# Kernel tuning notes

Measured on AMD Instinct MI355X. Metric: run time of the kernel, lower is better.

## Reference

```python
import jax, jax.numpy as jnp
import numpy as np

V, D, H, KV, L, FF, HD = 32000, 768, 12, 4, 4, 2048, 64
N_REP = H // KV  # 3
EPS = 1e-6
ROPE_THETA = 10000.0


def setup_inputs() -> dict:
    key = jax.random.key(0)
    ks = jax.random.split(key, 12)
    s = 0.02
    return {
        'idx': jax.random.randint(ks[0], (1, 2048), 0, V),
        'embed': jax.random.normal(ks[1], (V, D), jnp.float32) * s,
        'ln1_w': jnp.ones((L, D), jnp.float32),
        'Wq': jax.random.normal(ks[2], (L, D, H * HD), jnp.float32) * s,
        'Wk': jax.random.normal(ks[3], (L, D, KV * HD), jnp.float32) * s,
        'Wv': jax.random.normal(ks[4], (L, D, KV * HD), jnp.float32) * s,
        'Wo': jax.random.normal(ks[5], (L, H * HD, D), jnp.float32) * s,
        'ln2_w': jnp.ones((L, D), jnp.float32),
        'Wg': jax.random.normal(ks[6], (L, D, FF), jnp.float32) * s,
        'Wu': jax.random.normal(ks[7], (L, D, FF), jnp.float32) * s,
        'Wd': jax.random.normal(ks[8], (L, FF, D), jnp.float32) * s,
        'normf_w': jnp.ones((D,), jnp.float32),
    }


def _rms(x, w):
    xf = x.astype(jnp.float32)
    var = jnp.mean(xf * xf, axis=-1, keepdims=True)
    return w * (xf * jax.lax.rsqrt(var + EPS)).astype(x.dtype)


def _rotate_half(x):
    x1, x2 = x[..., : x.shape[-1] // 2], x[..., x.shape[-1] // 2:]
    return jnp.concatenate((-x2, x1), axis=-1)


def reference(idx, embed, ln1_w, Wq, Wk, Wv, Wo, ln2_w, Wg, Wu, Wd, normf_w):
    B, T = idx.shape
    x = embed[idx]  # [B,T,D]

    # RoPE tables: cos/sin [1,1,T,HD]
    inv_freq = 1.0 / (ROPE_THETA ** (jnp.arange(0, HD, 2, dtype=jnp.float32) / HD))
    pos = jnp.arange(T, dtype=jnp.float32)
    freqs = pos[:, None] * inv_freq[None, :]          # [T,HD/2]
    emb = jnp.concatenate((freqs, freqs), axis=-1)     # [T,HD]
    cos = jnp.cos(emb)[None, None].astype(x.dtype)
    sin = jnp.sin(emb)[None, None].astype(x.dtype)

    causal = jnp.tril(jnp.ones((T, T), bool))[None, None]  # [1,1,T,T]
    scale = 1.0 / np.sqrt(HD)

    for l in range(L):
        # --- attention ---
        h = _rms(x, ln1_w[l])
        q = (h @ Wq[l]).reshape(B, T, H, HD).transpose(0, 2, 1, 3)   # [B,H,T,HD]
        k = (h @ Wk[l]).reshape(B, T, KV, HD).transpose(0, 2, 1, 3)  # [B,KV,T,HD]
        v = (h @ Wv[l]).reshape(B, T, KV, HD).transpose(0, 2, 1, 3)
        q = q * cos + _rotate_half(q) * sin
        k = k * cos + _rotate_half(k) * sin
        k = jnp.repeat(k, N_REP, axis=1)  # [B,H,T,HD]
        v = jnp.repeat(v, N_REP, axis=1)
        scores = jnp.einsum('bhqd,bhkd->bhqk', q, k) * scale
        scores = jnp.where(causal, scores, -jnp.inf)
        probs = jax.nn.softmax(scores.astype(jnp.float32), axis=-1).astype(q.dtype)
        attn = jnp.einsum('bhqk,bhkd->bhqd', probs, v)
        attn = attn.transpose(0, 2, 1, 3).reshape(B, T, H * HD)
        x = x + attn @ Wo[l]
        # --- gated MLP ---
        h = _rms(x, ln2_w[l])
        x = x + (jax.nn.gelu(h @ Wg[l], approximate=True) * (h @ Wu[l])) @ Wd[l]

    x = _rms(x, normf_w)
    logits = (x @ embed.T).astype(jnp.float32)  # tied lm_head
    return logits
```

## Files before the change

### kernel.cpp

```cpp
#include <hip/hip_runtime.h>

#define TSEQ 2048
#define DM   768
#define NH   12
#define NKV  4
#define HD   64
#define FFD  2048
#define NL   4
#define VOC  32000
#define QKVN 1280

typedef __attribute__((ext_vector_type(8))) short short8;
typedef __attribute__((ext_vector_type(4))) float f32x4;

__device__ __forceinline__ unsigned short f2b(float f) {
  unsigned int u = __float_as_uint(f);
  u += 0x7fffu + ((u >> 16) & 1u);
  return (unsigned short)(u >> 16);
}
__device__ __forceinline__ float b2f(unsigned short u) {
  return __uint_as_float(((unsigned int)u) << 16);
}
__device__ __forceinline__ unsigned int packbf(float a, float b) {
  return (unsigned int)f2b(a) | ((unsigned int)f2b(b) << 16);
}

__device__ __forceinline__ void gl16(const unsigned short* g, unsigned short* l) {
  __builtin_amdgcn_global_load_lds(
      (const __attribute__((address_space(1))) void*)g,
      (__attribute__((address_space(3))) void*)l, 16, 0, 0);
}

__global__ void cast_bf16_kernel(const float* __restrict__ src,
                                 unsigned short* __restrict__ dst, int n4) {
  int i = blockIdx.x * blockDim.x + threadIdx.x;
  if (i >= n4) return;
  float4 v = ((const float4*)src)[i];
  uint2 o; o.x = packbf(v.x, v.y); o.y = packbf(v.z, v.w);
  ((uint2*)dst)[i] = o;
}

__global__ void rope_tab_kernel(float2* __restrict__ tab) {
  int i = blockIdx.x * blockDim.x + threadIdx.x;
  int pos = i >> 5, d = i & 31;
  float inv = exp2f(-(float)d * (13.287712379549449f / 32.0f));
  float sv, cv; sincosf((float)pos * inv, &sv, &cv);
  tab[i] = make_float2(cv, sv);
}

__global__ void transpose_cast_kernel(const float* __restrict__ src,
                                      unsigned short* __restrict__ dst,
                                      int K, int N, size_t sstride, size_t dstride) {
  __shared__ float tile[32][33];
  src += (size_t)blockIdx.z * sstride;
  dst += (size_t)blockIdx.z * dstride;
  int n0 = blockIdx.x * 32, k0 = blockIdx.y * 32;
  int tx = threadIdx.x, ty = threadIdx.y;
  #pragma unroll
  for (int i = 0; i < 4; ++i) {
    int r = ty + i * 8;
    tile[r][tx] = src[(size_t)(k0 + r) * N + n0 + tx];
  }
  __syncthreads();
  #pragma unroll
  for (int i = 0; i < 4; ++i) {
    int r = ty + i * 8;
    dst[(size_t)(n0 + r) * K + k0 + tx] = f2b(tile[tx][r]);
  }
}

__global__ void gather_kernel(const int* __restrict__ idx,
                              const float* __restrict__ embed,
                              float* __restrict__ x) {
  int row = blockIdx.x; int t = threadIdx.x;
  int id = idx[row];
  ((float4*)(x + (size_t)row * DM))[t] = ((const float4*)(embed + (size_t)id * DM))[t];
}

__global__ void rmsnorm_kernel(const float* __restrict__ x,
                               const float* __restrict__ w,
                               unsigned short* __restrict__ out) {
  int row = blockIdx.x; int t = threadIdx.x;
  const float* xr = x + (size_t)row * DM;
  float v0 = xr[t], v1 = xr[t + 256], v2 = xr[t + 512];
  float s = v0*v0 + v1*v1 + v2*v2;
  #pragma unroll
  for (int off = 1; off < 64; off <<= 1) s += __shfl_xor(s, off);
  __shared__ float red[4];
  if ((t & 63) == 0) red[t >> 6] = s;
  __syncthreads();
  float tot = red[0] + red[1] + red[2] + red[3];
  float rs = rsqrtf(tot * (1.0f / DM) + 1e-6f);
  unsigned short* orow = out + (size_t)row * DM;
  orow[t]       = f2b(w[t]       * v0 * rs);
  orow[t + 256] = f2b(w[t + 256] * v1 * rs);
  orow[t + 512] = f2b(w[t + 512] * v2 * rs);
}

__global__ __launch_bounds__(512, 1) void gemm_l8_kernel(
    const unsigned short* __restrict__ A, const unsigned short* __restrict__ Bt,
    float* __restrict__ C, int N, int K) {
  __shared__ unsigned short lds[2][2][256 * 64];
  const int NT = K >> 6;
  int bid = blockIdx.x, nwg = gridDim.x;
  int wgid = (bid & 7) * (nwg >> 3) + (bid >> 3);
  int m0 = (wgid & 7) * 256;
  int n0 = (wgid >> 3) * 256;
  int tid = threadIdx.x;
  int lane = tid & 63, w = tid >> 6;
  int wm = w >> 2, wn = w & 3;
  int al = lane & 15, ag = lane >> 4;
  int swz = (al & 7) << 3;

  int rA = tid >> 3;
  int cK = ((tid & 7) * 8) ^ ((rA & 7) << 3);
  const unsigned short* Ag = A + (size_t)(m0 + rA) * K + cK;
  const unsigned short* Bg = Bt + (size_t)(n0 + rA) * K + cK;

  f32x4 acc[8][4];
  #pragma unroll
  for (int i = 0; i < 8; ++i)
    #pragma unroll
    for (int n = 0; n < 4; ++n) acc[i][n] = (f32x4){0.f, 0.f, 0.f, 0.f};

  #define STAGE(kt, c) { \
    size_t ko = (size_t)(kt) * 64; \
    unsigned short* dA = &lds[(c)][0][0] + w * 512; \
    unsigned short* dB = &lds[(c)][1][0] + w * 512; \
    gl16(Ag + (size_t)0   * K + ko, dA);            \
    gl16(Ag + (size_t)64  * K + ko, dA + 4096);     \
    gl16(Ag + (size_t)128 * K + ko, dA + 8192);     \
    gl16(Ag + (size_t)192 * K + ko, dA + 12288);    \
    gl16(Bg + (size_t)0   * K + ko, dB);            \
    gl16(Bg + (size_t)64  * K + ko, dB + 4096);     \
    gl16(Bg + (size_t)128 * K + ko, dB + 8192);     \
    gl16(Bg + (size_t)192 * K + ko, dB + 12288);    \
  }

  STAGE(0, 0);
  STAGE(1, 1);
  asm volatile("s_waitcnt vmcnt(8)" ::: "memory");
  __builtin_amdgcn_s_barrier();

  for (int t = 0; t < NT; ++t) {
    int cur = t & 1;
    const unsigned short* La = &lds[cur][0][0];
    const unsigned short* Lb = &lds[cur][1][0];
    short8 a0[8], b0[4], a1[8], b1[4];
    #pragma unroll
    for (int i = 0; i < 8; ++i)
      a0[i] = *(const short8*)&La[(wm*128 + i*16 + al)*64 + ((ag*8) ^ swz)];
    #pragma unroll
    for (int n = 0; n < 4; ++n)
      b0[n] = *(const short8*)&Lb[(wn*64 + n*16 + al)*64 + ((ag*8) ^ swz)];
    #pragma unroll
    for (int i = 0; i < 8; ++i)
      #pragma unroll
      for (int n = 0; n < 4; ++n)
        acc[i][n] = __builtin_amdgcn_mfma_f32_16x16x32_bf16(a0[i], b0[n], acc[i][n], 0, 0, 0);
    #pragma unroll
    for (int i = 0; i < 8; ++i)
      a1[i] = *(const short8*)&La[(wm*128 + i*16 + al)*64 + ((32 + ag*8) ^ swz)];
    #pragma unroll
    for (int n = 0; n < 4; ++n)
      b1[n] = *(const short8*)&Lb[(wn*64 + n*16 + al)*64 + ((32 + ag*8) ^ swz)];
    asm volatile("s_waitcnt lgkmcnt(0)" ::: "memory");
    __builtin_amdgcn_s_barrier();
    if (t + 2 < NT) STAGE(t + 2, cur);
    __builtin_amdgcn_s_setprio(1);
    #pragma unroll
    for (int i = 0; i < 8; ++i)
      #pragma unroll
      for (int n = 0; n < 4; ++n)
        acc[i][n] = __builtin_amdgcn_mfma_f32_16x16x32_bf16(a1[i], b1[n], acc[i][n], 0, 0, 0);
    __builtin_amdgcn_s_setprio(0);
    if (t + 2 < NT) { asm volatile("s_waitcnt vmcnt(8)" ::: "memory"); }
    else            { asm volatile("s_waitcnt vmcnt(0)" ::: "memory"); }
    __builtin_amdgcn_s_barrier();
  }
  #undef STAGE

  #pragma unroll
  for (int i = 0; i < 8; ++i)
    #pragma unroll
    for (int r = 0; r < 4; ++r) {
      float* Cr = C + (size_t)(m0 + wm*128 + i*16 + ag*4 + r) * N + n0 + wn*64 + al;
      #pragma unroll
      for (int n = 0; n < 4; ++n) Cr[n * 16] = acc[i][n][r];
    }
}

__global__ __launch_bounds__(512) void gemm_p8_kernel(
    const unsigned short* __restrict__ A, const unsigned short* __restrict__ Bt,
    float* __restrict__ C, int N, int K, int Kc) {
  __shared__ unsigned short lds[2][2][128 * 64];
  const int NT = Kc >> 6;
  int bid = blockIdx.x, nwg = gridDim.x;
  int wgid = (bid & 7) * (nwg >> 3) + (bid >> 3);
  int m0 = (wgid & 15) * 128;
  int n0 = (wgid >> 4) * 128;
  int tid = threadIdx.x;
  int lane = tid & 63, w = tid >> 6;
  int wm = w >> 2, wn = w & 3;
  int al = lane & 15, ag = lane >> 4;
  int swz = (al & 7) << 3;

  size_t koff = (size_t)blockIdx.y * Kc;
  int rp = 8 * w + (lane >> 3);
  int cK = ((lane & 7) * 8) ^ ((lane >> 3) << 3);
  const unsigned short* Ag = A + (size_t)(m0 + rp) * K + koff + cK;
  const unsigned short* Bg = Bt + (size_t)(n0 + rp) * K + koff + cK;

  f32x4 acc[4][2];
  #pragma unroll
  for (int i = 0; i < 4; ++i)
    #pragma unroll
    for (int n = 0; n < 2; ++n) acc[i][n] = (f32x4){0.f, 0.f, 0.f, 0.f};

  #define STAGE(kt, c) { \
    size_t ko = (size_t)(kt) * 64; \
    unsigned short* dA = &lds[(c)][0][0] + w * 512; \
    unsigned short* dB = &lds[(c)][1][0] + w * 512; \
    gl16(Ag + ko,                 dA);        \
    gl16(Ag + (size_t)64*K + ko,  dA + 4096); \
    gl16(Bg + ko,                 dB);        \
    gl16(Bg + (size_t)64*K + ko,  dB + 4096); \
  }

  STAGE(0, 0);
  STAGE(1, 1);
  asm volatile("s_waitcnt vmcnt(4)" ::: "memory");
  __builtin_amdgcn_s_barrier();

  for (int t = 0; t < NT; ++t) {
    int cur = t & 1;
    const unsigned short* La = &lds[cur][0][0];
    const unsigned short* Lb = &lds[cur][1][0];
    short8 a0[4], b0[2], a1[4], b1[2];
    #pragma unroll
    for (int i = 0; i < 4; ++i)
      a0[i] = *(const short8*)&La[(wm*64 + i*16 + al)*64 + ((ag*8) ^ swz)];
    #pragma unroll
    for (int n = 0; n < 2; ++n)
      b0[n] = *(const short8*)&Lb[(wn*32 + n*16 + al)*64 + ((ag*8) ^ swz)];
    #pragma unroll
    for (int i = 0; i < 4; ++i)
      #pragma unroll
      for (int n = 0; n < 2; ++n)
        acc[i][n] = __builtin_amdgcn_mfma_f32_16x16x32_bf16(a0[i], b0[n], acc[i][n], 0, 0, 0);
    #pragma unroll
    for (int i = 0; i < 4; ++i)
      a1[i] = *(const short8*)&La[(wm*64 + i*16 + al)*64 + ((32 + ag*8) ^ swz)];
    #pragma unroll
    for (int n = 0; n < 2; ++n)
      b1[n] = *(const short8*)&Lb[(wn*32 + n*16 + al)*64 + ((32 + ag*8) ^ swz)];
    asm volatile("s_waitcnt lgkmcnt(0)" ::: "memory");
    __builtin_amdgcn_s_barrier();
    if (t + 2 < NT) STAGE(t + 2, cur);
    __builtin_amdgcn_s_setprio(1);
    #pragma unroll
    for (int i = 0; i < 4; ++i)
      #pragma unroll
      for (int n = 0; n < 2; ++n)
        acc[i][n] = __builtin_amdgcn_mfma_f32_16x16x32_bf16(a1[i], b1[n], acc[i][n], 0, 0, 0);
    __builtin_amdgcn_s_setprio(0);
    if (t + 2 < NT) { asm volatile("s_waitcnt vmcnt(4)" ::: "memory"); }
    else            { asm volatile("s_waitcnt vmcnt(0)" ::: "memory"); }
    __builtin_amdgcn_s_barrier();
  }
  #undef STAGE

  #pragma unroll
  for (int i = 0; i < 4; ++i)
    #pragma unroll
    for (int r = 0; r < 4; ++r) {
      float* Cr = C + (size_t)(m0 + wm*64 + i*16 + ag*4 + r) * N + n0 + wn*32 + al;
      #pragma unroll
      for (int n = 0; n < 2; ++n) atomicAdd(&Cr[n * 16], acc[i][n][r]);
    }
}

__device__ __forceinline__ float gelu_t(float x) {
  float x3 = x * x * x;
  return 0.5f * x * (1.0f + tanhf(0.7978845608028654f * (x + 0.044715f * x3)));
}

__global__ __launch_bounds__(512) void gemm_gu8_kernel(
    const unsigned short* __restrict__ A, const unsigned short* __restrict__ BtG,
    const unsigned short* __restrict__ BtU, unsigned short* __restrict__ Cm) {
  __shared__ unsigned short lds[2][3][128 * 64];
  const int K = DM;
  const int NT = K >> 6;
  int bid = blockIdx.x, nwg = gridDim.x;
  int wgid = (bid & 7) * (nwg >> 3) + (bid >> 3);
  int m0 = (wgid & 15) * 128;
  int n0 = (wgid >> 4) * 128;
  int tid = threadIdx.x;
  int lane = tid & 63, w = tid >> 6;
  int wm = w >> 2, wn = w & 3;
  int al = lane & 15, ag = lane >> 4;
  int swz = (al & 7) << 3;

  int rp = 8 * w + (lane >> 3);
  int cK = ((lane & 7) * 8) ^ ((lane >> 3) << 3);
  const unsigned short* Ag = A + (size_t)(m0 + rp) * K + cK;
  const unsigned short* Gg = BtG + (size_t)(n0 + rp) * K + cK;
  const unsigned short* Ug = BtU + (size_t)(n0 + rp) * K + cK;

  f32x4 accg[4][2], accu[4][2];
  #pragma unroll
  for (int i = 0; i < 4; ++i)
    #pragma unroll
    for (int n = 0; n < 2; ++n) {
      accg[i][n] = (f32x4){0.f, 0.f, 0.f, 0.f};
      accu[i][n] = (f32x4){0.f, 0.f, 0.f, 0.f};
    }

  #define STAGE(kt, c) { \
    size_t ko = (size_t)(kt) * 64; \
    unsigned short* dA = &lds[(c)][0][0] + w * 512; \
    unsigned short* dG = &lds[(c)][1][0] + w * 512; \
    unsigned short* dU = &lds[(c)][2][0] + w * 512; \
    gl16(Ag + ko,                 dA);        \
    gl16(Ag + (size_t)64*K + ko,  dA + 4096); \
    gl16(Gg + ko,                 dG);        \
    gl16(Gg + (size_t)64*K + ko,  dG + 4096); \
    gl16(Ug + ko,                 dU);        \
    gl16(Ug + (size_t)64*K + ko,  dU + 4096); \
  }

  STAGE(0, 0);
  STAGE(1, 1);
  asm volatile("s_waitcnt vmcnt(6)" ::: "memory");
  __builtin_amdgcn_s_barrier();

  for (int t = 0; t < NT; ++t) {
    int cur = t & 1;
    const unsigned short* La = &lds[cur][0][0];
    const unsigned short* Lg = &lds[cur][1][0];
    const unsigned short* Lu = &lds[cur][2][0];
    short8 a0[4], g0[2], u0[2], a1[4], g1[2], u1[2];
    #pragma unroll
    for (int i = 0; i < 4; ++i)
      a0[i] = *(const short8*)&La[(wm*64 + i*16 + al)*64 + ((ag*8) ^ swz)];
    #pragma unroll
    for (int n = 0; n < 2; ++n) {
      g0[n] = *(const short8*)&Lg[(wn*32 + n*16 + al)*64 + ((ag*8) ^ swz)];
      u0[n] = *(const short8*)&Lu[(wn*32 + n*16 + al)*64 + ((ag*8) ^ swz)];
    }
    #pragma unroll
    for (int i = 0; i < 4; ++i)
      #pragma unroll
      for (int n = 0; n < 2; ++n) {
        accg[i][n] = __builtin_amdgcn_mfma_f32_16x16x32_bf16(a0[i], g0[n], accg[i][n], 0, 0, 0);
        accu[i][n] = __builtin_amdgcn_mfma_f32_16x16x32_bf16(a0[i], u0[n], accu[i][n], 0, 0, 0);
      }
    #pragma unroll
    for (int i = 0; i < 4; ++i)
      a1[i] = *(const short8*)&La[(wm*64 + i*16 + al)*64 + ((32 + ag*8) ^ swz)];
    #pragma unroll
    for (int n = 0; n < 2; ++n) {
      g1[n] = *(const short8*)&Lg[(wn*32 + n*16 + al)*64 + ((32 + ag*8) ^ swz)];
      u1[n] = *(const short8*)&Lu[(wn*32 + n*16 + al)*64 + ((32 + ag*8) ^ swz)];
    }
    asm volatile("s_waitcnt lgkmcnt(0)" ::: "memory");
    __builtin_amdgcn_s_barrier();
    if (t + 2 < NT) STAGE(t + 2, cur);
    __builtin_amdgcn_s_setprio(1);
    #pragma unroll
    for (int i = 0; i < 4; ++i)
      #pragma unroll
      for (int n = 0; n < 2; ++n) {
        accg[i][n] = __builtin_amdgcn_mfma_f32_16x16x32_bf16(a1[i], g1[n], accg[i][n], 0, 0, 0);
        accu[i][n] = __builtin_amdgcn_mfma_f32_16x16x32_bf16(a1[i], u1[n], accu[i][n], 0, 0, 0);
      }
    __builtin_amdgcn_s_setprio(0);
    if (t + 2 < NT) { asm volatile("s_waitcnt vmcnt(6)" ::: "memory"); }
    else            { asm volatile("s_waitcnt vmcnt(0)" ::: "memory"); }
    __builtin_amdgcn_s_barrier();
  }
  #undef STAGE

  #pragma unroll
  for (int i = 0; i < 4; ++i)
    #pragma unroll
    for (int r = 0; r < 4; ++r) {
      unsigned short* Cr = Cm + (size_t)(m0 + wm*64 + i*16 + ag*4 + r) * FFD + n0 + wn*32 + al;
      #pragma unroll
      for (int n = 0; n < 2; ++n)
        Cr[n * 16] = f2b(gelu_t(accg[i][n][r]) * accu[i][n][r]);
    }
}

__global__ __launch_bounds__(256) void gemm_qkv_kernel(
    const unsigned short* __restrict__ A, const unsigned short* __restrict__ Bt,
    unsigned short* __restrict__ C, unsigned short* __restrict__ vT,
    const float2* __restrict__ rope_tab) {
  const int N = QKVN, K = DM;
  __shared__ unsigned short As[128 * 40];
  __shared__ unsigned short Bs[128 * 40];
  int bid = blockIdx.x, nwg = gridDim.x;
  int wgid = (bid & 7) * (nwg >> 3) + (bid >> 3);
  int m0 = (wgid & 15) * 128;
  int n0 = (wgid >> 4) * 128;
  int tid = threadIdx.x;
  int lane = tid & 63, wave = tid >> 6;
  int wr = (wave >> 1) * 64, wc = (wave & 1) * 64;
  int l16 = lane & 15, lk8 = (lane >> 4) * 8;
  f32x4 acc[4][4];
  #pragma unroll
  for (int m = 0; m < 4; ++m)
    #pragma unroll
    for (int n = 0; n < 4; ++n) acc[m][n] = (f32x4){0.f, 0.f, 0.f, 0.f};
  const unsigned short* Abase = A + (size_t)m0 * K;
  const unsigned short* Bbase = Bt + (size_t)n0 * K;
  int r0 = tid >> 2;
  int c0 = (tid & 3) * 8;
  for (int k0 = 0; k0 < K; k0 += 32) {
    uint4 a0 = *(const uint4*)(Abase + (size_t)r0 * K + k0 + c0);
    uint4 a1 = *(const uint4*)(Abase + (size_t)(r0 + 64) * K + k0 + c0);
    uint4 b0 = *(const uint4*)(Bbase + (size_t)r0 * K + k0 + c0);
    uint4 b1 = *(const uint4*)(Bbase + (size_t)(r0 + 64) * K + k0 + c0);
    *(uint4*)&As[r0 * 40 + c0] = a0;
    *(uint4*)&As[(r0 + 64) * 40 + c0] = a1;
    *(uint4*)&Bs[r0 * 40 + c0] = b0;
    *(uint4*)&Bs[(r0 + 64) * 40 + c0] = b1;
    __syncthreads();
    short8 af[4], bfr[4];
    #pragma unroll
    for (int m = 0; m < 4; ++m) af[m]  = *(const short8*)&As[(wr + m*16 + l16) * 40 + lk8];
    #pragma unroll
    for (int n = 0; n < 4; ++n) bfr[n] = *(const short8*)&Bs[(wc + n*16 + l16) * 40 + lk8];
    #pragma unroll
    for (int m = 0; m < 4; ++m)
      #pragma unroll
      for (int n = 0; n < 4; ++n)
        acc[m][n] = __builtin_amdgcn_mfma_f32_16x16x32_bf16(af[m], bfr[n], acc[m][n], 0, 0, 0);
    __syncthreads();
  }
  bool qk = (n0 + wc) < 1024;
  #pragma unroll
  for (int m = 0; m < 4; ++m)
    #pragma unroll
    for (int r = 0; r < 4; ++r) {
      int pos = m0 + wr + m*16 + ((lane >> 4) << 2) + r;
      if (qk) {
        unsigned short* Cr = C + (size_t)pos * N + n0 + wc + l16;
        #pragma unroll
        for (int n = 0; n < 2; ++n) {
          int d = n * 16 + l16;
          float2 cs = rope_tab[pos * 32 + d];
          float x1 = acc[m][n][r], x2 = acc[m][n + 2][r];
          Cr[n * 16]       = f2b(x1 * cs.x - x2 * cs.y);
          Cr[(n + 2) * 16] = f2b(x2 * cs.x + x1 * cs.y);
        }
      } else {
        #pragma unroll
        for (int n = 0; n < 4; ++n) {
          int hb = n0 + wc + n*16 + l16 - 1024;
          vT[(size_t)hb * TSEQ + pos] = f2b(acc[m][n][r]);
        }
      }
    }
}

__global__ __launch_bounds__(256) void attn_chunk_kernel(
    const unsigned short* __restrict__ qkv, const unsigned short* __restrict__ vT,
    unsigned short* __restrict__ out, float* __restrict__ pO, float* __restrict__ pML) {
  __shared__ unsigned short Ks[2][64 * 64];
  __shared__ unsigned short Vt[2][64 * 64];
  __shared__ unsigned short Ps[4][16 * 64];
  int s = blockIdx.x, h = blockIdx.y;
  int qt, ci;
  if (s < 8)       { qt = s;                ci = 0; }
  else if (s < 24) { qt = 8 + ((s-8) >> 1); ci = (s-8) & 1; }
  else if (s < 48) { qt = 16 + (s-24) / 3;  ci = (s-24) % 3; }
  else             { qt = 24 + ((s-48) >> 2); ci = (s-48) & 3; }
  int nt = qt + 1;
  int t0 = ci * 8;
  int t1 = t0 + 8; if (t1 > nt) t1 = nt;
  int cnt = (nt + 7) >> 3;
  int r0 = qt * 64;
  int kvh = h / 3;
  int t = threadIdx.x;
  int lane = t & 63, w = t >> 6;
  int l16 = lane & 15, g = lane >> 4;

  int qr = r0 + w * 16 + l16;
  const unsigned short* qrow = qkv + (size_t)qr * QKVN + h * HD;
  short8 aq0 = *(const short8*)(qrow + 8 * g);
  short8 aq1 = *(const short8*)(qrow + 32 + 8 * g);

  int sw = (lane & 7) ^ (lane >> 3);
  int rloc = w * 16 + (lane >> 3);
  const unsigned short* kgb = qkv + (size_t)rloc * QKVN + DM + kvh * HD + 8 * sw;
  const unsigned short* vgb = vT + (size_t)(kvh * 64 + rloc) * TSEQ + 8 * sw;

  #define ASTAGE(kb, c) { \
    unsigned short* kd = &Ks[(c)][0] + w * 1024; \
    unsigned short* vd = &Vt[(c)][0] + w * 1024; \
    gl16(kgb + (size_t)(kb) * QKVN,       kd);       \
    gl16(kgb + (size_t)((kb) + 8) * QKVN, kd + 512); \
    gl16(vgb + (kb),                      vd);       \
    gl16(vgb + (size_t)8 * TSEQ + (kb),   vd + 512); \
  }

  f32x4 o_acc[4];
  float mrun[4], lsum[4];
  #pragma unroll
  for (int i = 0; i < 4; ++i) { o_acc[i] = (f32x4){0.f,0.f,0.f,0.f}; mrun[i] = -1e30f; lsum[i] = 0.f; }

  ASTAGE(t0 * 64, 0);
  for (int kt = t0; kt < t1; ++kt) {
    int cur = (kt - t0) & 1;
    int kb = kt * 64;
    if (kt + 1 < t1) {
      ASTAGE((kt + 1) * 64, cur ^ 1);
      asm volatile("s_waitcnt vmcnt(4)" ::: "memory");
    } else {
      asm volatile("s_waitcnt vmcnt(0)" ::: "memory");
    }
    __builtin_amdgcn_s_barrier();

    const unsigned short* Kc = &Ks[cur][0];
    const unsigned short* Vc = &Vt[cur][0];

    f32x4 s_acc[4];
    #pragma unroll
    for (int nb = 0; nb < 4; ++nb) s_acc[nb] = (f32x4){0.f,0.f,0.f,0.f};
    #pragma unroll
    for (int nb = 0; nb < 4; ++nb) {
      int key = nb * 16 + l16;
      short8 bk0 = *(const short8*)&Kc[key * 64 + ((g       ^ (key & 7)) << 3)];
      short8 bk1 = *(const short8*)&Kc[key * 64 + (((4 + g) ^ (key & 7)) << 3)];
      s_acc[nb] = __builtin_amdgcn_mfma_f32_16x16x32_bf16(aq0, bk0, s_acc[nb], 0, 0, 0);
      s_acc[nb] = __builtin_amdgcn_mfma_f32_16x16x32_bf16(aq1, bk1, s_acc[nb], 0, 0, 0);
    }

    bool diag = (kt == qt);
    #pragma unroll
    for (int r = 0; r < 4; ++r) {
      int qg = r0 + w * 16 + g * 4 + r;
      float sv[4];
      #pragma unroll
      for (int nb = 0; nb < 4; ++nb) {
        sv[nb] = s_acc[nb][r] * 0.125f;
        if (diag && (kb + nb * 16 + l16 > qg)) sv[nb] = -1e30f;
      }
      float mx = fmaxf(fmaxf(sv[0], sv[1]), fmaxf(sv[2], sv[3]));
      mx = fmaxf(mx, __shfl_xor(mx, 1));
      mx = fmaxf(mx, __shfl_xor(mx, 2));
      mx = fmaxf(mx, __shfl_xor(mx, 4));
      mx = fmaxf(mx, __shfl_xor(mx, 8));
      if (mx > mrun[r] + 8.0f) {
        float es = __expf(mrun[r] - mx);
        lsum[r] *= es;
        #pragma unroll
        for (int db = 0; db < 4; ++db) o_acc[db][r] *= es;
        mrun[r] = mx;
      }
      float rsum = 0.f;
      #pragma unroll
      for (int nb = 0; nb < 4; ++nb) { sv[nb] = __expf(sv[nb] - mrun[r]); rsum += sv[nb]; }
      lsum[r] += rsum;
      int qloc = g * 4 + r, q7 = qloc & 7;
      #pragma unroll
      for (int nb = 0; nb < 4; ++nb) {
        int key = nb * 16 + l16;
        Ps[w][qloc * 64 + ((((key >> 3) ^ q7) << 3) + (key & 7))] = f2b(sv[nb]);
      }
    }

    #pragma unroll
    for (int kc = 0; kc < 2; ++kc) {
      short8 pa = *(const short8*)&Ps[w][l16 * 64 + (((4 * kc + g) ^ (l16 & 7)) << 3)];
      #pragma unroll
      for (int db = 0; db < 4; ++db) {
        int d = db * 16 + l16;
        short8 bv = *(const short8*)&Vc[d * 64 + (((4 * kc + g) ^ (d & 7)) << 3)];
        o_acc[db] = __builtin_amdgcn_mfma_f32_16x16x32_bf16(pa, bv, o_acc[db], 0, 0, 0);
      }
    }
    __builtin_amdgcn_s_barrier();
  }
  #undef ASTAGE

  if (cnt == 1) {
    #pragma unroll
    for (int r = 0; r < 4; ++r) {
      int qg = r0 + w * 16 + g * 4 + r;
      float sr = lsum[r];
      sr += __shfl_xor(sr, 1);
      sr += __shfl_xor(sr, 2);
      sr += __shfl_xor(sr, 4);
      sr += __shfl_xor(sr, 8);
      float inv = 1.0f / sr;
      unsigned short* orow = out + (size_t)qg * DM + h * HD + l16;
      #pragma unroll
      for (int db = 0; db < 4; ++db) orow[db * 16] = f2b(o_acc[db][r] * inv);
    }
  } else {
    size_t slotg = (size_t)h * 80 + s;
    float* po = pO + slotg * 4096;
    float* pm = pML + slotg * 128;
    #pragma unroll
    for (int r = 0; r < 4; ++r) {
      int row = w * 16 + g * 4 + r;
      float sr = lsum[r];
      sr += __shfl_xor(sr, 1);
      sr += __shfl_xor(sr, 2);
      sr += __shfl_xor(sr, 4);
      sr += __shfl_xor(sr, 8);
      #pragma unroll
      for (int db = 0; db < 4; ++db) po[row * 64 + db * 16 + l16] = o_acc[db][r];
      if (l16 == 0) { pm[row * 2] = mrun[r]; pm[row * 2 + 1] = sr; }
    }
  }
}

__global__ __launch_bounds__(256) void attn_combine_kernel(
    const float* __restrict__ pO, const float* __restrict__ pML,
    unsigned short* __restrict__ out) {
  int h = blockIdx.y;
  int qt = 8 + blockIdx.x;
  int base, cnt;
  if (qt < 16)      { base = 8 + (qt - 8) * 2;  cnt = 2; }
  else if (qt < 24) { base = 24 + (qt - 16) * 3; cnt = 3; }
  else              { base = 48 + (qt - 24) * 4; cnt = 4; }
  int t = threadIdx.x;
  int row = t >> 2, d0 = (t & 3) * 16;
  float m[4], l[4];
  float M = -1e30f;
  for (int c = 0; c < cnt; ++c) {
    const float* pm = pML + ((size_t)h * 80 + base + c) * 128 + row * 2;
    m[c] = pm[0]; l[c] = pm[1];
    M = fmaxf(M, m[c]);
  }
  float o[16];
  #pragma unroll
  for (int j = 0; j < 16; ++j) o[j] = 0.f;
  float wl = 0.f;
  for (int c = 0; c < cnt; ++c) {
    float wc = __expf(m[c] - M);
    wl += wc * l[c];
    const float4* po = (const float4*)(pO + ((size_t)h * 80 + base + c) * 4096 + row * 64 + d0);
    #pragma unroll
    for (int q = 0; q < 4; ++q) {
      float4 v = po[q];
      o[q*4+0] += wc * v.x; o[q*4+1] += wc * v.y;
      o[q*4+2] += wc * v.z; o[q*4+3] += wc * v.w;
    }
  }
  float inv = 1.0f / wl;
  unsigned short* orow = out + (size_t)(qt * 64 + row) * DM + h * HD + d0;
  uint4 s0, s1;
  s0.x = packbf(o[0]*inv,  o[1]*inv);  s0.y = packbf(o[2]*inv,  o[3]*inv);
  s0.z = packbf(o[4]*inv,  o[5]*inv);  s0.w = packbf(o[6]*inv,  o[7]*inv);
  s1.x = packbf(o[8]*inv,  o[9]*inv);  s1.y = packbf(o[10]*inv, o[11]*inv);
  s1.z = packbf(o[12]*inv, o[13]*inv); s1.w = packbf(o[14]*inv, o[15]*inv);
  ((uint4*)orow)[0] = s0; ((uint4*)orow)[1] = s1;
}

extern "C" void kernel_launch(void* const* d_in, const int* in_sizes, int n_in,
                              void* d_out, int out_size, void* d_ws, size_t ws_size,
                              hipStream_t stream) {
  const int*   idx   = (const int*)d_in[0];
  const float* embed = (const float*)d_in[1];
  const float* ln1   = (const float*)d_in[2];
  const float* Wq    = (const float*)d_in[3];
  const float* Wk    = (const float*)d_in[4];
  const float* Wv    = (const float*)d_in[5];
  const float* Wo    = (const float*)d_in[6];
  const float* ln2   = (const float*)d_in[7];
  const float* Wg    = (const float*)d_in[8];
  const float* Wu    = (const float*)d_in[9];
  const float* Wd    = (const float*)d_in[10];
  const float* normf = (const float*)d_in[11];
  float* out = (float*)d_out;
  char* ws = (char*)d_ws;
  (void)in_sizes; (void)n_in; (void)out_size; (void)ws_size;

  unsigned short* embed_bf = (unsigned short*)ws;
  size_t off = (size_t)VOC * DM * 2;
  unsigned short* wts = (unsigned short*)(ws + off);
  const size_t LW = (size_t)QKVN * DM + (size_t)DM * DM
                  + 2ull * FFD * DM + (size_t)DM * FFD;
  off += LW * 2ull * NL;
  float* xf = (float*)(ws + off);            off += (size_t)TSEQ * DM * 4;
  unsigned short* h_bf = (unsigned short*)(ws + off);    off += (size_t)TSEQ * DM * 2;
  unsigned short* qkv_bf = (unsigned short*)(ws + off);  off += (size_t)TSEQ * QKVN * 2;
  unsigned short* attn_bf = (unsigned short*)(ws + off); off += (size_t)TSEQ * DM * 2;
  float* pO = (float*)(ws + off);
  unsigned short* m_bf = (unsigned short*)(ws + off);
  off += (size_t)NH * 80 * 4096 * 4;
  float* pML = (float*)(ws + off);           off += (size_t)NH * 80 * 128 * 4;
  float2* rope_tab = (float2*)(ws + off);    off += (size_t)TSEQ * 32 * 8;
  unsigned short* vT = (unsigned short*)(ws + off);      off += (size_t)NKV * HD * TSEQ * 2;

  cast_bf16_kernel<<<(VOC * DM / 4 + 255) / 256, 256, 0, stream>>>(embed, embed_bf, VOC * DM / 4);
  rope_tab_kernel<<<TSEQ * 32 / 256, 256, 0, stream>>>(rope_tab);

  {
    unsigned short* qkvT = wts;
    unsigned short* woT  = wts + (size_t)QKVN * DM;
    unsigned short* wguT = woT + (size_t)DM * DM;
    unsigned short* wdT  = wguT + 2ull * FFD * DM;
    transpose_cast_kernel<<<dim3(24, 24, NL), dim3(32, 8), 0, stream>>>(Wq, qkvT, 768, 768, 589824, LW);
    transpose_cast_kernel<<<dim3(8, 24, NL),  dim3(32, 8), 0, stream>>>(Wk, qkvT + 768ull * 768, 768, 256, 196608, LW);
    transpose_cast_kernel<<<dim3(8, 24, NL),  dim3(32, 8), 0, stream>>>(Wv, qkvT + 1024ull * 768, 768, 256, 196608, LW);
    transpose_cast_kernel<<<dim3(24, 24, NL), dim3(32, 8), 0, stream>>>(Wo, woT, 768, 768, 589824, LW);
    transpose_cast_kernel<<<dim3(64, 24, NL), dim3(32, 8), 0, stream>>>(Wg, wguT, 768, 2048, 1572864, LW);
    transpose_cast_kernel<<<dim3(64, 24, NL), dim3(32, 8), 0, stream>>>(Wu, wguT + (size_t)FFD * DM, 768, 2048, 1572864, LW);
    transpose_cast_kernel<<<dim3(24, 64, NL), dim3(32, 8), 0, stream>>>(Wd, wdT, 2048, 768, 1572864, LW);
  }

  gather_kernel<<<TSEQ, 192, 0, stream>>>(idx, embed, xf);

  for (int l = 0; l < NL; ++l) {
    unsigned short* base = wts + (size_t)l * LW;
    unsigned short* qkvT = base;
    unsigned short* woT  = base + (size_t)QKVN * DM;
    unsigned short* wguT = woT + (size_t)DM * DM;
    unsigned short* wdT  = wguT + 2ull * FFD * DM;

    rmsnorm_kernel<<<TSEQ, 256, 0, stream>>>(xf, ln1 + (size_t)l * DM, h_bf);
    gemm_qkv_kernel<<<(QKVN / 128) * 16, 256, 0, stream>>>(h_bf, qkvT, qkv_bf, vT, rope_tab);
    attn_chunk_kernel<<<dim3(80, NH), 256, 0, stream>>>(qkv_bf, vT, attn_bf, pO, pML);
    attn_combine_kernel<<<dim3(24, NH), 256, 0, stream>>>(pO, pML, attn_bf);
    gemm_p8_kernel<<<dim3((DM / 128) * 16, 3), 512, 0, stream>>>(attn_bf, woT, xf, DM, DM, 256);
    rmsnorm_kernel<<<TSEQ, 256, 0, stream>>>(xf, ln2 + (size_t)l * DM, h_bf);
    gemm_gu8_kernel<<<(FFD / 128) * 16, 512, 0, stream>>>(h_bf, wguT, wguT + (size_t)FFD * DM, m_bf);
    gemm_p8_kernel<<<dim3((DM / 128) * 16, 4), 512, 0, stream>>>(m_bf, wdT, xf, DM, FFD, 512);
  }

  rmsnorm_kernel<<<TSEQ, 256, 0, stream>>>(xf, normf, h_bf);
  gemm_l8_kernel<<<(VOC / 256) * (TSEQ / 256), 512, 0, stream>>>(h_bf, embed_bf, out, VOC, DM);
}
```

Measured before the change: 769.8 us.

## Merge weight transpose launches and interleave LDS fragment loads with MFMA

Seven per-matrix transpose-cast launches become one kernel that works out which matrix each block handles from its flat block index, which saves launch overhead. The three GEMM kernels' inner loops are reordered so the second half-tile's LDS fragment loads are issued before the first half's MFMAs, with partial lgkmcnt waits and sched_barriers. This is meant to hide LDS latency behind matrix math. It raises register pressure because more fragments are live at once.

```diff
diff --git a/kernel.cpp b/kernel.cpp
--- a/kernel.cpp
+++ b/kernel.cpp
@@ -48,24 +48,39 @@
   tab[i] = make_float2(cv, sv);
 }
 
-__global__ void transpose_cast_kernel(const float* __restrict__ src,
-                                      unsigned short* __restrict__ dst,
-                                      int K, int N, size_t sstride, size_t dstride) {
+__global__ void transpose_all_kernel(const float* __restrict__ Wq, const float* __restrict__ Wk,
+                                     const float* __restrict__ Wv, const float* __restrict__ Wo,
+                                     const float* __restrict__ Wg, const float* __restrict__ Wu,
+                                     const float* __restrict__ Wd, unsigned short* __restrict__ wts,
+                                     size_t LW) {
   __shared__ float tile[32][33];
-  src += (size_t)blockIdx.z * sstride;
-  dst += (size_t)blockIdx.z * dstride;
-  int n0 = blockIdx.x * 32, k0 = blockIdx.y * 32;
+  int r = blockIdx.x, l = blockIdx.z;
+  const float* src; size_t sstr, doff; int K, N, nx;
+  if (r < 576)       { src = Wq; sstr = 589824;  doff = 0;                          K = 768;  N = 768;  nx = 24; }
+  else if (r < 768)  { src = Wk; sstr = 196608;  doff = 768ull * 768;               K = 768;  N = 256;  nx = 8;  r -= 576; }
+  else if (r < 960)  { src = Wv; sstr = 196608;  doff = 1024ull * 768;              K = 768;  N = 256;  nx = 8;  r -= 768; }
+  else if (r < 1536) { src = Wo; sstr = 589824;  doff = (size_t)QKVN * DM;          K = 768;  N = 768;  nx = 24; r -= 960; }
+  else if (r < 3072) { src = Wg; sstr = 1572864; doff = (size_t)QKVN * DM + (size_t)DM * DM;
+                       K = 768;  N = 2048; nx = 64; r -= 1536; }
+  else if (r < 4608) { src = Wu; sstr = 1572864; doff = (size_t)QKVN * DM + (size_t)DM * DM + (size_t)FFD * DM;
+                       K = 768;  N = 2048; nx = 64; r -= 3072; }
+  else               { src = Wd; sstr = 1572864; doff = (size_t)QKVN * DM + (size_t)DM * DM + 2ull * FFD * DM;
+                       K = 2048; N = 768;  nx = 24; r -= 4608; }
+  int bx = r % nx, by = r / nx;
+  src += (size_t)l * sstr;
+  unsigned short* dst = wts + (size_t)l * LW + doff;
+  int n0 = bx * 32, k0 = by * 32;
   int tx = threadIdx.x, ty = threadIdx.y;
   #pragma unroll
   for (int i = 0; i < 4; ++i) {
-    int r = ty + i * 8;
-    tile[r][tx] = src[(size_t)(k0 + r) * N + n0 + tx];
+    int rr = ty + i * 8;
+    tile[rr][tx] = src[(size_t)(k0 + rr) * N + n0 + tx];
   }
   __syncthreads();
   #pragma unroll
   for (int i = 0; i < 4; ++i) {
-    int r = ty + i * 8;
-    dst[(size_t)(n0 + r) * K + k0 + tx] = f2b(tile[tx][r]);
+    int rr = ty + i * 8;
+    dst[(size_t)(n0 + rr) * K + k0 + tx] = f2b(tile[tx][rr]);
   }
 }
 
@@ -148,28 +163,51 @@
     const unsigned short* Lb = &lds[cur][1][0];
     short8 a0[8], b0[4], a1[8], b1[4];
     #pragma unroll
-    for (int i = 0; i < 8; ++i)
+    for (int i = 0; i < 4; ++i)
       a0[i] = *(const short8*)&La[(wm*128 + i*16 + al)*64 + ((ag*8) ^ swz)];
     #pragma unroll
     for (int n = 0; n < 4; ++n)
       b0[n] = *(const short8*)&Lb[(wn*64 + n*16 + al)*64 + ((ag*8) ^ swz)];
     #pragma unroll
-    for (int i = 0; i < 8; ++i)
+    for (int i = 4; i < 8; ++i)
+      a0[i] = *(const short8*)&La[(wm*128 + i*16 + al)*64 + ((ag*8) ^ swz)];
+    asm volatile("s_waitcnt lgkmcnt(4)" ::: "memory");
+    __builtin_amdgcn_sched_barrier(0);
+    #pragma unroll
+    for (int i = 0; i < 4; ++i)
       #pragma unroll
       for (int n = 0; n < 4; ++n)
         acc[i][n] = __builtin_amdgcn_mfma_f32_16x16x32_bf16(a0[i], b0[n], acc[i][n], 0, 0, 0);
     #pragma unroll
-    for (int i = 0; i < 8; ++i)
-      a1[i] = *(const short8*)&La[(wm*128 + i*16 + al)*64 + ((32 + ag*8) ^ swz)];
-    #pragma unroll
     for (int n = 0; n < 4; ++n)
       b1[n] = *(const short8*)&Lb[(wn*64 + n*16 + al)*64 + ((32 + ag*8) ^ swz)];
+    #pragma unroll
+    for (int i = 0; i < 4; ++i)
+      a1[i] = *(const short8*)&La[(wm*128 + i*16 + al)*64 + ((32 + ag*8) ^ swz)];
+    asm volatile("s_waitcnt lgkmcnt(8)" ::: "memory");
+    __builtin_amdgcn_sched_barrier(0);
+    #pragma unroll
+    for (int i = 4; i < 8; ++i)
+      #pragma unroll
+      for (int n = 0; n < 4; ++n)
+        acc[i][n] = __builtin_amdgcn_mfma_f32_16x16x32_bf16(a0[i], b0[n], acc[i][n], 0, 0, 0);
+    #pragma unroll
+    for (int i = 4; i < 8; ++i)
+      a1[i] = *(const short8*)&La[(wm*128 + i*16 + al)*64 + ((32 + ag*8) ^ swz)];
+    asm volatile("s_waitcnt lgkmcnt(4)" ::: "memory");
+    __builtin_amdgcn_sched_barrier(0);
+    #pragma unroll
+    for (int i = 0; i < 4; ++i)
+      #pragma unroll
+      for (int n = 0; n < 4; ++n)
+        acc[i][n] = __builtin_amdgcn_mfma_f32_16x16x32_bf16(a1[i], b1[n], acc[i][n], 0, 0, 0);
     asm volatile("s_waitcnt lgkmcnt(0)" ::: "memory");
+    __builtin_amdgcn_sched_barrier(0);
     __builtin_amdgcn_s_barrier();
     if (t + 2 < NT) STAGE(t + 2, cur);
     __builtin_amdgcn_s_setprio(1);
     #pragma unroll
-    for (int i = 0; i < 8; ++i)
+    for (int i = 4; i < 8; ++i)
       #pragma unroll
       for (int n = 0; n < 4; ++n)
         acc[i][n] = __builtin_amdgcn_mfma_f32_16x16x32_bf16(a1[i], b1[n], acc[i][n], 0, 0, 0);
@@ -245,16 +283,19 @@
       b0[n] = *(const short8*)&Lb[(wn*32 + n*16 + al)*64 + ((ag*8) ^ swz)];
     #pragma unroll
     for (int i = 0; i < 4; ++i)
+      a1[i] = *(const short8*)&La[(wm*64 + i*16 + al)*64 + ((32 + ag*8) ^ swz)];
+    #pragma unroll
+    for (int n = 0; n < 2; ++n)
+      b1[n] = *(const short8*)&Lb[(wn*32 + n*16 + al)*64 + ((32 + ag*8) ^ swz)];
+    asm volatile("s_waitcnt lgkmcnt(6)" ::: "memory");
+    __builtin_amdgcn_sched_barrier(0);
+    #pragma unroll
+    for (int i = 0; i < 4; ++i)
       #pragma unroll
       for (int n = 0; n < 2; ++n)
         acc[i][n] = __builtin_amdgcn_mfma_f32_16x16x32_bf16(a0[i], b0[n], acc[i][n], 0, 0, 0);
-    #pragma unroll
-    for (int i = 0; i < 4; ++i)
-      a1[i] = *(const short8*)&La[(wm*64 + i*16 + al)*64 + ((32 + ag*8) ^ swz)];
-    #pragma unroll
-    for (int n = 0; n < 2; ++n)
-      b1[n] = *(const short8*)&Lb[(wn*32 + n*16 + al)*64 + ((32 + ag*8) ^ swz)];
     asm volatile("s_waitcnt lgkmcnt(0)" ::: "memory");
+    __builtin_amdgcn_sched_barrier(0);
     __builtin_amdgcn_s_barrier();
     if (t + 2 < NT) STAGE(t + 2, cur);
     __builtin_amdgcn_s_setprio(1);
@@ -350,20 +391,23 @@
     }
     #pragma unroll
     for (int i = 0; i < 4; ++i)
+      a1[i] = *(const short8*)&La[(wm*64 + i*16 + al)*64 + ((32 + ag*8) ^ swz)];
+    #pragma unroll
+    for (int n = 0; n < 2; ++n) {
+      g1[n] = *(const short8*)&Lg[(wn*32 + n*16 + al)*64 + ((32 + ag*8) ^ swz)];
+      u1[n] = *(const short8*)&Lu[(wn*32 + n*16 + al)*64 + ((32 + ag*8) ^ swz)];
+    }
+    asm volatile("s_waitcnt lgkmcnt(8)" ::: "memory");
+    __builtin_amdgcn_sched_barrier(0);
+    #pragma unroll
+    for (int i = 0; i < 4; ++i)
       #pragma unroll
       for (int n = 0; n < 2; ++n) {
         accg[i][n] = __builtin_amdgcn_mfma_f32_16x16x32_bf16(a0[i], g0[n], accg[i][n], 0, 0, 0);
         accu[i][n] = __builtin_amdgcn_mfma_f32_16x16x32_bf16(a0[i], u0[n], accu[i][n], 0, 0, 0);
       }
-    #pragma unroll
-    for (int i = 0; i < 4; ++i)
-      a1[i] = *(const short8*)&La[(wm*64 + i*16 + al)*64 + ((32 + ag*8) ^ swz)];
-    #pragma unroll
-    for (int n = 0; n < 2; ++n) {
-      g1[n] = *(const short8*)&Lg[(wn*32 + n*16 + al)*64 + ((32 + ag*8) ^ swz)];
-      u1[n] = *(const short8*)&Lu[(wn*32 + n*16 + al)*64 + ((32 + ag*8) ^ swz)];
-    }
     asm volatile("s_waitcnt lgkmcnt(0)" ::: "memory");
+    __builtin_amdgcn_sched_barrier(0);
     __builtin_amdgcn_s_barrier();
     if (t + 2 < NT) STAGE(t + 2, cur);
     __builtin_amdgcn_s_setprio(1);
@@ -699,20 +743,8 @@
 
   cast_bf16_kernel<<<(VOC * DM / 4 + 255) / 256, 256, 0, stream>>>(embed, embed_bf, VOC * DM / 4);
   rope_tab_kernel<<<TSEQ * 32 / 256, 256, 0, stream>>>(rope_tab);
-
-  {
-    unsigned short* qkvT = wts;
-    unsigned short* woT  = wts + (size_t)QKVN * DM;
-    unsigned short* wguT = woT + (size_t)DM * DM;
-    unsigned short* wdT  = wguT + 2ull * FFD * DM;
-    transpose_cast_kernel<<<dim3(24, 24, NL), dim3(32, 8), 0, stream>>>(Wq, qkvT, 768, 768, 589824, LW);
-    transpose_cast_kernel<<<dim3(8, 24, NL),  dim3(32, 8), 0, stream>>>(Wk, qkvT + 768ull * 768, 768, 256, 196608, LW);
-    transpose_cast_kernel<<<dim3(8, 24, NL),  dim3(32, 8), 0, stream>>>(Wv, qkvT + 1024ull * 768, 768, 256, 196608, LW);
-    transpose_cast_kernel<<<dim3(24, 24, NL), dim3(32, 8), 0, stream>>>(Wo, woT, 768, 768, 589824, LW);
-    transpose_cast_kernel<<<dim3(64, 24, NL), dim3(32, 8), 0, stream>>>(Wg, wguT, 768, 2048, 1572864, LW);
-    transpose_cast_kernel<<<dim3(64, 24, NL), dim3(32, 8), 0, stream>>>(Wu, wguT + (size_t)FFD * DM, 768, 2048, 1572864, LW);
-    transpose_cast_kernel<<<dim3(24, 64, NL), dim3(32, 8), 0, stream>>>(Wd, wdT, 2048, 768, 1572864, LW);
-  }
+  transpose_all_kernel<<<dim3(6144, 1, NL), dim3(32, 8), 0, stream>>>(
+      Wq, Wk, Wv, Wo, Wg, Wu, Wd, wts, LW);
 
   gather_kernel<<<TSEQ, 192, 0, stream>>>(idx, embed, xf);
 
```

Result: no change. 760.6 us (-1.2%).
